# Kernel tuning notes

Measured on AMD Instinct MI355X. Metric: run time of the kernel, lower is better.

## Reference

```python
import jax, jax.numpy as jnp
import numpy as np

BQ, LQ, BD, LD, TOK_D, CLS_D = 64, 32, 128, 192, 32, 768
VOCAB = 5000

def setup_inputs() -> dict:
    key = jax.random.key(0)
    ks = jax.random.split(key, 6)
    return {
        "query_tok_embs": jax.random.normal(ks[0], (BQ, LQ, TOK_D), dtype=jnp.float32),
        "doc_tok_embs": jax.random.normal(ks[1], (BD, LD, TOK_D), dtype=jnp.float32),
        "query_cls_emb": jax.random.normal(ks[2], (BQ, CLS_D), dtype=jnp.float32),
        "doc_cls_emb": jax.random.normal(ks[3], (BD, CLS_D), dtype=jnp.float32),
        "query_input_ids": jax.random.randint(ks[4], (BQ, LQ), 0, VOCAB, dtype=jnp.int64 if jax.config.jax_enable_x64 else jnp.int32).astype(jnp.int32),
        "doc_input_ids": jax.random.randint(ks[5], (BD, LD), 0, VOCAB, dtype=jnp.int64 if jax.config.jax_enable_x64 else jnp.int32).astype(jnp.int32),
        "query_attention_mask": jnp.ones((BQ, LQ), dtype=jnp.int32),
    }

def _mask_sep(attention_mask):
    # zero out the [SEP] position (last attended token) per query
    sep_pos = attention_mask.sum(axis=1) - 1          # [Bq]
    rows = jnp.arange(attention_mask.shape[0])
    return attention_mask.at[rows, sep_pos].set(0)

def reference(query_tok_embs, doc_tok_embs, query_cls_emb, doc_cls_emb,
              query_input_ids, doc_input_ids, query_attention_mask):
    qmask = _mask_sep(query_attention_mask).astype(query_tok_embs.dtype)  # [Bq, Lq]
    # cartesian token similarity: [Bq, Lq, Bd, Ld]
    scores = jnp.einsum('qie,dje->qidj', query_tok_embs, doc_tok_embs)
    # exact token-id match mask; scores * match.float() == where(match, scores, 0)
    match = query_input_ids[:, :, None, None] == doc_input_ids[None, None, :, :]
    masked = jnp.where(match, scores, jnp.zeros((), scores.dtype))
    tok = masked.max(axis=-1)                          # [Bq, Lq, Bd] max over doc positions
    tok_scores = (tok * qmask[:, :, None])[:, 1:, :].sum(axis=1)  # drop CLS pos, sum over query toks
    cls_scores = query_cls_emb @ doc_cls_emb.T         # [Bq, Bd]
    return tok_scores + cls_scores
```

## Files before the change

### kernel.cpp

```cpp
#include <hip/hip_runtime.h>

#define BQ 64
#define LQ 32
#define BD 128
#define LD 192
#define TOK_D 32
#define CLS_D 768

__global__ __launch_bounds__(256) void coil_kernel(
    const float* __restrict__ qtok,
    const float* __restrict__ dtok,
    const float* __restrict__ qcls,
    const float* __restrict__ dcls,
    const int*   __restrict__ qids,
    const int*   __restrict__ dids,
    const int*   __restrict__ qatt,
    float*       __restrict__ out)
{
    const int blk = blockIdx.x;
    const int q = blk >> 7;
    const int d = blk & (BD - 1);
    const int t = threadIdx.x;

    __shared__ int   s_qid[LQ];
    __shared__ int   s_att[LQ];
    __shared__ int   s_did[LD];
    __shared__ float s_tok[LQ];
    __shared__ float s_red[4];

    if (t < LQ) {
        s_qid[t] = qids[q * LQ + t];
        s_att[t] = qatt[q * LQ + t];
    }
    if (t < LD) {
        s_did[t] = dids[d * LD + t];
    }
    __syncthreads();

    const int i = t >> 3;
    const int k = t & 7;
    const float* qrow = qtok + (q * LQ + i) * TOK_D;
    const int myqid = s_qid[i];
    float lmax = -INFINITY;
    for (int j = k; j < LD; j += 8) {
        float val = 0.0f;
        if (s_did[j] == myqid) {
            const float* drow = dtok + (d * LD + j) * TOK_D;
            float acc = 0.0f;
            #pragma unroll
            for (int e = 0; e < TOK_D; ++e) acc = fmaf(qrow[e], drow[e], acc);
            val = acc;
        }
        lmax = fmaxf(lmax, val);
    }
    lmax = fmaxf(lmax, __shfl_xor(lmax, 1));
    lmax = fmaxf(lmax, __shfl_xor(lmax, 2));
    lmax = fmaxf(lmax, __shfl_xor(lmax, 4));
    if (k == 0) s_tok[i] = lmax;

    float part = 0.0f;
    {
        const float* qc = qcls + q * CLS_D;
        const float* dc = dcls + d * CLS_D;
        for (int c = t; c < CLS_D; c += 256) part = fmaf(qc[c], dc[c], part);
    }
    #pragma unroll
    for (int off = 32; off >= 1; off >>= 1) part += __shfl_xor(part, off);
    if ((t & 63) == 0) s_red[t >> 6] = part;
    __syncthreads();

    if (t == 0) {
        int msum = 0;
        #pragma unroll
        for (int ii = 0; ii < LQ; ++ii) msum += s_att[ii];
        const int sep = msum - 1;
        float tsum = 0.0f;
        for (int ii = 1; ii < LQ; ++ii) {
            const float m = (ii == sep) ? 0.0f : (float)s_att[ii];
            tsum += s_tok[ii] * m;
        }
        const float cls = s_red[0] + s_red[1] + s_red[2] + s_red[3];
        out[q * BD + d] = tsum + cls;
    }
}

extern "C" void kernel_launch(void* const* d_in, const int* in_sizes, int n_in,
                              void* d_out, int out_size, void* d_ws, size_t ws_size,
                              hipStream_t stream) {
    const float* qtok = (const float*)d_in[0];
    const float* dtok = (const float*)d_in[1];
    const float* qcls = (const float*)d_in[2];
    const float* dcls = (const float*)d_in[3];
    const int*   qids = (const int*)d_in[4];
    const int*   dids = (const int*)d_in[5];
    const int*   qatt = (const int*)d_in[6];
    float* out = (float*)d_out;

    coil_kernel<<<BQ * BD, 256, 0, stream>>>(qtok, dtok, qcls, dcls,
                                             qids, dids, qatt, out);
}
```

Baseline: 89.62 us.

## Shrink blocks to one wavefront with vectorized loads and shuffle-only reduction

Each (query, doc) block now runs as a single 64-thread wavefront instead of 256 threads. Two lanes share each query token, and ids and embeddings are read as int4/float4 vectors. Non-matching positions no longer compute anything: a flag applies the zero floor once at the end. The final token and CLS reduction moves from a serial thread-0 loop into a full-wave shuffle reduction. The aim is to cut block overhead, synchronisation cost and scalar loads. In exchange each lane does more serial work over doc positions, and per-CU occupancy changes.

```diff
diff --git a/kernel.cpp b/kernel.cpp
--- a/kernel.cpp
+++ b/kernel.cpp
@@ -7,7 +7,7 @@
 #define TOK_D 32
 #define CLS_D 768
 
-__global__ __launch_bounds__(256) void coil_kernel(
+__global__ __launch_bounds__(64) void coil_kernel(
     const float* __restrict__ qtok,
     const float* __restrict__ dtok,
     const float* __restrict__ qcls,
@@ -22,66 +22,87 @@
     const int d = blk & (BD - 1);
     const int t = threadIdx.x;
 
+    __shared__ int   s_did[LD];
     __shared__ int   s_qid[LQ];
     __shared__ int   s_att[LQ];
-    __shared__ int   s_did[LD];
     __shared__ float s_tok[LQ];
-    __shared__ float s_red[4];
 
-    if (t < LQ) {
-        s_qid[t] = qids[q * LQ + t];
-        s_att[t] = qatt[q * LQ + t];
-    }
-    if (t < LD) {
-        s_did[t] = dids[d * LD + t];
+    if (t < 48) {
+        ((int4*)s_did)[t] = ((const int4*)(dids + d * LD))[t];
+    } else if (t < 56) {
+        ((int4*)s_qid)[t - 48] = ((const int4*)(qids + q * LQ))[t - 48];
+    } else {
+        ((int4*)s_att)[t - 56] = ((const int4*)(qatt + q * LQ))[t - 56];
     }
     __syncthreads();
 
-    const int i = t >> 3;
-    const int k = t & 7;
-    const float* qrow = qtok + (q * LQ + i) * TOK_D;
+    const int i = t >> 1;
+    const int k = t & 1;
     const int myqid = s_qid[i];
+    const float4* qr = (const float4*)(qtok + (q * LQ + i) * TOK_D);
+
     float lmax = -INFINITY;
-    for (int j = k; j < LD; j += 8) {
-        float val = 0.0f;
-        if (s_did[j] == myqid) {
-            const float* drow = dtok + (d * LD + j) * TOK_D;
-            float acc = 0.0f;
-            #pragma unroll
-            for (int e = 0; e < TOK_D; ++e) acc = fmaf(qrow[e], drow[e], acc);
-            val = acc;
+    bool hadZero = false;
+
+    auto dotj = [&](int j) -> float {
+        const float4* dr = (const float4*)(dtok + (d * LD + j) * TOK_D);
+        float acc = 0.0f;
+        #pragma unroll
+        for (int e = 0; e < TOK_D / 4; ++e) {
+            float4 a = qr[e], b = dr[e];
+            acc = fmaf(a.x, b.x, acc);
+            acc = fmaf(a.y, b.y, acc);
+            acc = fmaf(a.z, b.z, acc);
+            acc = fmaf(a.w, b.w, acc);
         }
-        lmax = fmaxf(lmax, val);
+        return acc;
+    };
+
+    for (int c = k; c < LD / 4; c += 2) {
+        const int4 ids = ((const int4*)s_did)[c];
+        const int j0 = c * 4;
+        if (ids.x == myqid) lmax = fmaxf(lmax, dotj(j0 + 0)); else hadZero = true;
+        if (ids.y == myqid) lmax = fmaxf(lmax, dotj(j0 + 1)); else hadZero = true;
+        if (ids.z == myqid) lmax = fmaxf(lmax, dotj(j0 + 2)); else hadZero = true;
+        if (ids.w == myqid) lmax = fmaxf(lmax, dotj(j0 + 3)); else hadZero = true;
     }
+    if (hadZero) lmax = fmaxf(lmax, 0.0f);
     lmax = fmaxf(lmax, __shfl_xor(lmax, 1));
-    lmax = fmaxf(lmax, __shfl_xor(lmax, 2));
-    lmax = fmaxf(lmax, __shfl_xor(lmax, 4));
     if (k == 0) s_tok[i] = lmax;
 
     float part = 0.0f;
     {
-        const float* qc = qcls + q * CLS_D;
-        const float* dc = dcls + d * CLS_D;
-        for (int c = t; c < CLS_D; c += 256) part = fmaf(qc[c], dc[c], part);
+        const float4* qc = (const float4*)(qcls + q * CLS_D);
+        const float4* dc = (const float4*)(dcls + d * CLS_D);
+        #pragma unroll
+        for (int r = 0; r < 3; ++r) {
+            float4 a = qc[t + 64 * r];
+            float4 b = dc[t + 64 * r];
+            part = fmaf(a.x, b.x, part);
+            part = fmaf(a.y, b.y, part);
+            part = fmaf(a.z, b.z, part);
+            part = fmaf(a.w, b.w, part);
+        }
+    }
+    __syncthreads();
+
+    const int att = s_att[t & 31];
+    int msum = att;
+    msum += __shfl_xor(msum, 1);
+    msum += __shfl_xor(msum, 2);
+    msum += __shfl_xor(msum, 4);
+    msum += __shfl_xor(msum, 8);
+    msum += __shfl_xor(msum, 16);
+    const int sep = msum - 1;
+
+    float tot = part;
+    if (t >= 1 && t < LQ) {
+        const float m = (t == sep) ? 0.0f : (float)att;
+        tot += s_tok[t] * m;
     }
     #pragma unroll
-    for (int off = 32; off >= 1; off >>= 1) part += __shfl_xor(part, off);
-    if ((t & 63) == 0) s_red[t >> 6] = part;
-    __syncthreads();
-
-    if (t == 0) {
-        int msum = 0;
-        #pragma unroll
-        for (int ii = 0; ii < LQ; ++ii) msum += s_att[ii];
-        const int sep = msum - 1;
-        float tsum = 0.0f;
-        for (int ii = 1; ii < LQ; ++ii) {
-            const float m = (ii == sep) ? 0.0f : (float)s_att[ii];
-            tsum += s_tok[ii] * m;
-        }
-        const float cls = s_red[0] + s_red[1] + s_red[2] + s_red[3];
-        out[q * BD + d] = tsum + cls;
-    }
+    for (int off = 1; off < 64; off <<= 1) tot += __shfl_xor(tot, off);
+    if (t == 0) out[q * BD + d] = tot;
 }
 
 extern "C" void kernel_launch(void* const* d_in, const int* in_sizes, int n_in,
@@ -96,6 +117,6 @@
     const int*   qatt = (const int*)d_in[6];
     float* out = (float*)d_out;
 
-    coil_kernel<<<BQ * BD, 256, 0, stream>>>(qtok, dtok, qcls, dcls,
-                                             qids, dids, qatt, out);
+    coil_kernel<<<BQ * BD, 64, 0, stream>>>(qtok, dtok, qcls, dcls,
+                                            qids, dids, qatt, out);
 }
```

Result: faster. 81.30 us (-9.3%).
